# Kernel optimization log

Hardware: AMD Instinct MI355X
Metric: run time of the kernel (lower is better)

Reference implementation:

```python
import jax, jax.numpy as jnp
import numpy as np

NHID, NHEAD, HEAD_DIM, U = 512, 16, 64, 3  # U = unfold_size (hardcoded 3 in original)
B, L = 8, 2048
D = NHEAD * HEAD_DIM  # 1024


def setup_inputs() -> dict:
    key = jax.random.key(0)
    ks = jax.random.split(key, 9)
    s = 0.02
    return {
        "x": jax.random.normal(ks[0], (B, NHID, L, 1), jnp.float32),
        "wq": jax.random.normal(ks[1], (NHID, D), jnp.float32) * s,
        "bq": jnp.zeros((D,), jnp.float32),
        "wk": jax.random.normal(ks[2], (NHID, D), jnp.float32) * s,
        "bk": jnp.zeros((D,), jnp.float32),
        "wv": jax.random.normal(ks[3], (NHID, D), jnp.float32) * s,
        "bv": jnp.zeros((D,), jnp.float32),
        "wo": jax.random.normal(ks[4], (D, NHID), jnp.float32) * s,
        "bo": jnp.zeros((NHID,), jnp.float32),
    }


def _unfold(t):
    # t: (B, D, L). Replicates tf.image.extract_patches (ksize 3, SAME, zero pad)
    # followed by the original's reshape (B,L,1,D,3) -- which reinterprets the
    # window-major flat layout (w*D + c) as (c', w') -- then transpose to
    # (B, D, 3, L) and reshape to (B, nhead, head_dim, 3, L).
    b, d, l = t.shape
    tt = jnp.transpose(t, (0, 2, 1))                  # (B, L, D)
    tp = jnp.pad(tt, ((0, 0), (1, 1), (0, 0)))        # SAME zero padding along L
    p = jnp.stack([tp[:, w:w + l, :] for w in range(U)], axis=2)  # (B, L, 3, D), flat idx = w*D + c
    p = p.reshape(b, l, d, U)                         # faithful reinterpreting reshape
    p = jnp.transpose(p, (0, 2, 3, 1))                # (B, D, 3, L)
    return p.reshape(b, NHEAD, HEAD_DIM, U, l)


def reference(x, wq, bq, wk, bk, wv, bv, wo, bo):
    b, c, l, _ = x.shape
    xs = x[..., 0]                                    # (B, C, L)
    # 1x1 convs (channels_first) == channel matmuls
    q = jnp.einsum('bcl,cd->bdl', xs, wq) + bq[None, :, None]
    k = jnp.einsum('bcl,cd->bdl', xs, wk) + bk[None, :, None]
    v = jnp.einsum('bcl,cd->bdl', xs, wv) + bv[None, :, None]
    q = q.reshape(b, NHEAD, HEAD_DIM, 1, l)           # (B, nh, hd, 1, L)
    k = _unfold(k)                                    # (B, nh, hd, 3, L)
    v = _unfold(v)
    scale = jnp.sqrt(jnp.asarray(HEAD_DIM, x.dtype))
    alphas = jnp.sum(q * k, axis=2, keepdims=True) / scale  # (B, nh, 1, 3, L)
    alphas = jax.nn.softmax(alphas, axis=3)
    att = jnp.sum(alphas * v, axis=3)                 # (B, nh, hd, L)
    # faithful to original: transpose then reinterpreting reshape to (B, D, L)
    att = jnp.transpose(att, (0, 1, 3, 2)).reshape(b, D, l)
    ret = jnp.einsum('bdl,dc->bcl', att, wo) + bo[None, :, None]
    return ret[..., None]                             # (B, nhid, L, 1)
```

## Files before the change

kernel.cpp:

```cpp
#include <hip/hip_runtime.h>

typedef _Float16 f16_t;
typedef _Float16 f16x2 __attribute__((ext_vector_type(2)));
typedef _Float16 f16x8 __attribute__((ext_vector_type(8)));
typedef float floatx4 __attribute__((ext_vector_type(4)));
typedef unsigned int u32;
typedef const __attribute__((address_space(1))) unsigned int* gptr_as1;
typedef __attribute__((address_space(3))) unsigned int* lptr_as3;

#define B_ 8
#define C_ 512
#define L_ 2048
#define D_ 1024
#define H_ 16

static __device__ __forceinline__ f16x2 bc2(u32 v) { return __builtin_bit_cast(f16x2, v); }
static __device__ __forceinline__ u32 cb2(f16x2 v) { return __builtin_bit_cast(u32, v); }

#define SCHEDB() __builtin_amdgcn_sched_barrier(0)

__global__ __launch_bounds__(256) void _MSA1_ktransf2h(const float* __restrict__ in,
                                                       f16_t* __restrict__ out,
                                                       int R, int C) {
  size_t zoff = (size_t)blockIdx.z * R * C;
  in += zoff; out += zoff;
  __shared__ f16_t tile[64][65];
  int r0 = blockIdx.y * 64, c0 = blockIdx.x * 64;
  int t = threadIdx.x;
  #pragma unroll
  for (int i = 0; i < 16; ++i) {
    int idx = t + i * 256;
    int r = idx >> 6, c = idx & 63;
    tile[c][r] = (f16_t)in[(size_t)(r0 + r) * C + (c0 + c)];
  }
  __syncthreads();
  #pragma unroll
  for (int i = 0; i < 16; ++i) {
    int idx = t + i * 256;
    int r = idx >> 6, c = idx & 63;
    out[(size_t)(c0 + r) * R + (r0 + c)] = tile[r][c];
  }
}

__global__ __launch_bounds__(256) void _MSA1_kprep(
    const float* __restrict__ wq, const float* __restrict__ wk,
    const float* __restrict__ wv, const float* __restrict__ wo,
    const float* __restrict__ bq, const float* __restrict__ bk,
    const float* __restrict__ bv,
    f16_t* __restrict__ wT3, f16_t* __restrict__ woT, float* __restrict__ bias3) {
  const int x = blockIdx.x, y = blockIdx.y;
  const int t = threadIdx.x;
  if (x == 128) {
    if (y == 0) {
      for (int i = t; i < 1024; i += 256) {
        bias3[i] = bq[i];
        bias3[1024 + i] = bk[i];
        bias3[2048 + i] = bv[i];
      }
    }
    return;
  }
  __shared__ f16_t tile[64][65];
  const float* in; f16_t* out; int R, C, r0, c0;
  if (y < 3) {
    R = 512; C = 1024;
    in = (y == 0) ? wq : (y == 1) ? wk : wv;
    out = wT3 + (size_t)y * 524288;
    r0 = (x >> 4) * 64; c0 = (x & 15) * 64;
  } else {
    R = 1024; C = 512;
    in = wo; out = woT;
    r0 = (x >> 3) * 64; c0 = (x & 7) * 64;
  }
  #pragma unroll
  for (int i = 0; i < 16; ++i) {
    int idx = t + i * 256;
    int r = idx >> 6, c = idx & 63;
    tile[c][r] = (f16_t)in[(size_t)(r0 + r) * C + (c0 + c)];
  }
  __syncthreads();
  #pragma unroll
  for (int i = 0; i < 16; ++i) {
    int idx = t + i * 256;
    int r = idx >> 6, c = idx & 63;
    out[(size_t)(c0 + r) * R + (r0 + c)] = tile[r][c];
  }
}

template <int K>
__global__ __launch_bounds__(512, 2) void _MSA1_kgemm8(
    const f16_t* __restrict__ A, const f16_t* __restrict__ Bt,
    const float* __restrict__ bias, f16_t* __restrict__ Cd0,
    int M, int N, long sB, long sC) {
  constexpr int KT = K / 64;
  int nx, my, zz;
  if (gridDim.z == 8) {
    const int o = blockIdx.x + 8 * (blockIdx.y + 12 * blockIdx.z);
    zz = o & 7; const int r = o >> 3; nx = r & 7; my = r >> 3;
  } else {
    nx = blockIdx.x; my = blockIdx.y; zz = blockIdx.z;
  }
  const f16_t* Bz = Bt + (size_t)zz * sB;
  const int m0 = my * 256, n0 = nx * 256;

  union __align__(16) ShU {
    f16_t AB[8][8192];
    f16_t Ep[64][264];
  };
  __shared__ ShU sh;

  const int t = threadIdx.x;
  const int lane = t & 63;
  const int wid = t >> 6;
  const int wm = wid & 1, wn = wid >> 1;
  const int mh = wm * 128, nh = wn * 64;
  const int fm = lane & 15, fq = lane >> 4;
  const int srcswz = ((t & 3) ^ ((t >> 2) & 3) ^ ((t >> 4) & 3)) * 8;
  const int colf = ((fq ^ (fm & 3) ^ ((fm >> 2) & 3)) * 8);

  floatx4 acc[8][4];
  #pragma unroll
  for (int i = 0; i < 8; ++i)
    #pragma unroll
    for (int j = 0; j < 4; ++j) {
      floatx4 z4 = {0.f, 0.f, 0.f, 0.f};
      acc[i][j] = z4;
    }

  auto SG = [&](int T, int ab, int kk) {
    const int d = T & 1;
    const f16_t* src = ab ? Bz : A;
    const int base0 = ab ? n0 : m0;
    char* ldsb = (char*)&sh.AB[(d * 2 + ab) * 2 + kk][0];
    #pragma unroll
    for (int j = 0; j < 2; ++j) {
      int idx = j * 512 + t;
      int r = idx >> 2;
      const f16_t* g = src + (size_t)(base0 + r) * K + T * 64 + kk * 32 + srcswz;
      __builtin_amdgcn_global_load_lds((gptr_as1)(const void*)g,
          (lptr_as3)(void*)(ldsb + idx * 16), 16, 0, 0);
    }
  };
  auto LDA4 = [&](f16x8* af, int d, int kk, int mhalf) {
    #pragma unroll
    for (int m2 = 0; m2 < 4; ++m2)
      af[m2] = *(const f16x8*)&sh.AB[(d * 2 + 0) * 2 + kk]
                  [(mh + mhalf * 64 + m2 * 16 + fm) * 32 + colf];
  };
  auto LDB4 = [&](f16x8* bf, int d, int kk) {
    #pragma unroll
    for (int nt = 0; nt < 4; ++nt)
      bf[nt] = *(const f16x8*)&sh.AB[(d * 2 + 1) * 2 + kk]
                  [(nh + nt * 16 + fm) * 32 + colf];
  };
  auto MM = [&](const f16x8* af, const f16x8* bf, int mhalf) {
    __builtin_amdgcn_s_setprio(1);
    #pragma unroll
    for (int m2 = 0; m2 < 4; ++m2)
      #pragma unroll
      for (int nt = 0; nt < 4; ++nt)
        acc[mhalf * 4 + m2][nt] = __builtin_amdgcn_mfma_f32_16x16x32_f16(
            af[m2], bf[nt], acc[mhalf * 4 + m2][nt], 0, 0, 0);
    __builtin_amdgcn_s_setprio(0);
  };

  SG(0, 1, 0); SG(0, 0, 0); SG(0, 1, 1); SG(0, 0, 1);
  SG(1, 1, 0); SG(1, 0, 0); SG(1, 1, 1);
  SCHEDB();
  asm volatile("s_waitcnt vmcnt(10)" ::: "memory");
  __builtin_amdgcn_s_barrier();
  SCHEDB();

  f16x8 af[4], bfr[4];
  #pragma unroll
  for (int i = 0; i < KT; ++i) {
    const int d = i & 1;
    LDB4(bfr, d, 0);
    LDA4(af, d, 0, 0);
    SCHEDB();
    __builtin_amdgcn_s_barrier();
    asm volatile("s_waitcnt lgkmcnt(0)" ::: "memory");
    SCHEDB();
    if (i + 1 < KT) SG(i + 1, 0, 1);
    MM(af, bfr, 0);
    LDA4(af, d, 0, 1);
    SCHEDB();
    if (i == KT - 1) {
      asm volatile("s_waitcnt vmcnt(0)" ::: "memory");
    } else {
      asm volatile("s_waitcnt vmcnt(8)" ::: "memory");
    }
    __builtin_amdgcn_s_barrier();
    asm volatile("s_waitcnt lgkmcnt(0)" ::: "memory");
    SCHEDB();
    if (i + 2 < KT) SG(i + 2, 1, 0);
    MM(af, bfr, 1);
    LDB4(bfr, d, 1);
    LDA4(af, d, 1, 0);
    SCHEDB();
    __builtin_amdgcn_s_barrier();
    asm volatile("s_waitcnt lgkmcnt(0)" ::: "memory");
    SCHEDB();
    if (i + 2 < KT) SG(i + 2, 0, 0);
    MM(af, bfr, 0);
    LDA4(af, d, 1, 1);
    SCHEDB();
    if (i + 1 < KT) {
      asm volatile("s_waitcnt vmcnt(8)" ::: "memory");
    }
    __builtin_amdgcn_s_barrier();
    asm volatile("s_waitcnt lgkmcnt(0)" ::: "memory");
    SCHEDB();
    if (i + 2 < KT) SG(i + 2, 1, 1);
    MM(af, bfr, 1);
  }
  __syncthreads();

  f16_t* Cd = Cd0 + (size_t)zz * sC;
  #pragma unroll
  for (int p = 0; p < 4; ++p) {
    if (p) __syncthreads();
    if (wm == (p >> 1)) {
      #pragma unroll
      for (int m2 = 0; m2 < 4; ++m2) {
        int mt = (p & 1) * 4 + m2;
        float bv4[4];
        #pragma unroll
        for (int r = 0; r < 4; ++r)
          bv4[r] = bias[m0 + p * 64 + m2 * 16 + fq * 4 + r];
        #pragma unroll
        for (int nt = 0; nt < 4; ++nt) {
          int col = nh + nt * 16 + fm;
          #pragma unroll
          for (int r = 0; r < 4; ++r) {
            int row = m2 * 16 + fq * 4 + r;
            sh.Ep[row][col] = (f16_t)(acc[mt][nt][r] + bv4[r]);
          }
        }
      }
    }
    __syncthreads();
    #pragma unroll
    for (int ii = 0; ii < 8; ++ii) {
      int chunk = ii * 512 + t;
      int row = chunk >> 6, c8 = chunk & 63;
      uint2 val = *(const uint2*)&sh.Ep[row][c8 * 4];
      *(uint2*)&Cd[(size_t)(m0 + p * 64 + row) * N + n0 + c8 * 4] = val;
    }
  }
}

template <bool F32OUT, int K>
__global__ __launch_bounds__(512, 2) void _MSA1_kgemm(
    const f16_t* __restrict__ A, const f16_t* __restrict__ Bt,
    const float* __restrict__ bias, void* __restrict__ Cdv,
    int M, int N, long sA, long sB, long sC) {
  int nx, my, zz;
  if (gridDim.z == 8) {
    const int o = blockIdx.x + 16 * (blockIdx.y + 2 * blockIdx.z);
    zz = o & 7; const int r = o >> 3; nx = r & 15; my = r >> 4;
  } else {
    nx = blockIdx.x; my = blockIdx.y; zz = blockIdx.z;
  }
  A  += (size_t)zz * sA;
  Bt += (size_t)zz * sB;
  const int m0 = my * 256, n0 = nx * 128;

  union __align__(16) ShU {
    struct { f16_t As[3][256][32]; f16_t Bs[3][128][32]; } ab;
    f16_t Ep[F32OUT ? 1 : 64][132];
  };
  __shared__ ShU sh;

  const int t = threadIdx.x;
  const int lane = t & 63, w = t >> 6;
  const int mh = (w & 3) * 64, nh = (w >> 2) * 64;
  const int fm = lane & 15, fq = lane >> 4;
  const int srcswz = ((t & 3) ^ ((t >> 2) & 3) ^ ((t >> 4) & 3)) * 8;
  const int colf = ((fq ^ (fm & 3) ^ ((fm >> 2) & 3)) * 8);

  floatx4 acc[4][4];
  #pragma unroll
  for (int i = 0; i < 4; ++i)
    #pragma unroll
    for (int j = 0; j < 4; ++j) {
      floatx4 z4 = {0.f, 0.f, 0.f, 0.f};
      acc[i][j] = z4;
    }

  auto STAGE = [&](int kt, int bi) {
    #pragma unroll
    for (int j = 0; j < 2; ++j) {
      int idx = j * 512 + t;
      int r = idx >> 2;
      const f16_t* ga = A + (size_t)(m0 + r) * K + kt + srcswz;
      __builtin_amdgcn_global_load_lds((gptr_as1)(const void*)ga,
          (lptr_as3)(void*)((char*)&sh.ab.As[bi][0][0] + j * 8192 + w * 1024), 16, 0, 0);
    }
    {
      int r = t >> 2;
      const f16_t* gb = Bt + (size_t)(n0 + r) * K + kt + srcswz;
      __builtin_amdgcn_global_load_lds((gptr_as1)(const void*)gb,
          (lptr_as3)(void*)((char*)&sh.ab.Bs[bi][0][0] + w * 1024), 16, 0, 0);
    }
  };

  STAGE(0, 0);
  STAGE(32, 1);
  SCHEDB();
  asm volatile("s_waitcnt vmcnt(3)" ::: "memory");
  __builtin_amdgcn_s_barrier();
  SCHEDB();

  int bcur = 0;
  for (int kt = 0; kt < K; kt += 32) {
    if (kt + 64 < K) {
      int bi = bcur + 2; if (bi >= 3) bi -= 3;
      STAGE(kt + 64, bi);
    }
    f16x8 af[4], bfr[4];
    #pragma unroll
    for (int mt = 0; mt < 4; ++mt)
      af[mt] = *(const f16x8*)&sh.ab.As[bcur][mh + mt * 16 + fm][colf];
    #pragma unroll
    for (int nt = 0; nt < 4; ++nt)
      bfr[nt] = *(const f16x8*)&sh.ab.Bs[bcur][nh + nt * 16 + fm][colf];
    __builtin_amdgcn_s_setprio(1);
    #pragma unroll
    for (int mt = 0; mt < 4; ++mt)
      #pragma unroll
      for (int nt = 0; nt < 4; ++nt)
        acc[mt][nt] = __builtin_amdgcn_mfma_f32_16x16x32_f16(
            af[mt], bfr[nt], acc[mt][nt], 0, 0, 0);
    __builtin_amdgcn_s_setprio(0);
    if (kt + 32 < K) {
      SCHEDB();
      if (kt + 64 < K)
        asm volatile("s_waitcnt vmcnt(3) lgkmcnt(0)" ::: "memory");
      else
        asm volatile("s_waitcnt vmcnt(0) lgkmcnt(0)" ::: "memory");
      __builtin_amdgcn_s_barrier();
      SCHEDB();
    }
    bcur = (bcur == 2) ? 0 : bcur + 1;
  }
  __syncthreads();

  if (F32OUT) {
    float* Cd = (float*)Cdv + (size_t)zz * sC;
    #pragma unroll
    for (int mt = 0; mt < 4; ++mt) {
      float bv4[4];
      #pragma unroll
      for (int r = 0; r < 4; ++r)
        bv4[r] = bias[m0 + mh + mt * 16 + fq * 4 + r];
      #pragma unroll
      for (int nt = 0; nt < 4; ++nt) {
        int col = n0 + nh + nt * 16 + fm;
        #pragma unroll
        for (int r = 0; r < 4; ++r) {
          int row = m0 + mh + mt * 16 + fq * 4 + r;
          Cd[(size_t)row * N + col] = acc[mt][nt][r] + bv4[r];
        }
      }
    }
  } else {
    f16_t* Cd = (f16_t*)Cdv + (size_t)zz * sC;
    #pragma unroll
    for (int p = 0; p < 4; ++p) {
      if (p) __syncthreads();
      if ((w & 1) == (p >> 1)) {
        #pragma unroll
        for (int mt2 = 0; mt2 < 4; ++mt2) {
          float bv4[4];
          #pragma unroll
          for (int r = 0; r < 4; ++r)
            bv4[r] = bias[m0 + p * 64 + mt2 * 16 + fq * 4 + r];
          #pragma unroll
          for (int nt = 0; nt < 4; ++nt) {
            int col = nh + nt * 16 + fm;
            #pragma unroll
            for (int r = 0; r < 4; ++r) {
              int row = mt2 * 16 + fq * 4 + r;
              sh.Ep[row & (F32OUT ? 0 : 63)][col] = (f16_t)(acc[mt2][nt][r] + bv4[r]);
            }
          }
        }
      }
      __syncthreads();
      #pragma unroll
      for (int i = 0; i < 8; ++i) {
        int chunk = i * 256 + (t & 255);
        int row = chunk >> 5, c8 = chunk & 31;
        uint2 val = *(const uint2*)&sh.Ep[row & (F32OUT ? 0 : 63)][c8 * 4];
        *(uint2*)&Cd[(size_t)(m0 + p * 64 + row) * N + n0 + c8 * 4] = val;
      }
    }
  }
}

__global__ __launch_bounds__(256) void _MSA1_kattn6(const f16_t* __restrict__ qkv,
                                                    f16_t* __restrict__ attT) {
  const int t = threadIdx.x;
  const int lane = t & 63;
  const int wid = __builtin_amdgcn_readfirstlane(t >> 6);
  const int hb = blockIdx.x;
  const int h = hb & 15, b = hb >> 4;
  const int chi = blockIdx.y;
  const int lbase = chi * 256;
  const int l0 = lbase + lane * 4;
  const size_t plane = (size_t)D_ * L_;
  const f16_t* base = qkv + (size_t)b * 3 * plane;

  __shared__ uint2 sred[4][3][64];
  __shared__ __align__(16) f16_t tile2[2048][8];

  const f16_t* qp = base + (size_t)(h * 64 + wid * 16) * L_ + l0;
  const f16_t* kpl = base + plane;
  const f16_t* vpl = base + 2 * plane;
  const int g0 = h * 192 + wid * 48;

  f16x2 sLo[3], sHi[3];
  #pragma unroll
  for (int w = 0; w < 3; ++w) { f16x2 z = {(f16_t)0, (f16_t)0}; sLo[w] = z; sHi[w] = z; }

  #pragma unroll
  for (int dd = 0; dd < 16; ++dd) {
    uint2 qw = *(const uint2*)(qp + (size_t)dd * L_);
    f16x2 qlo = bc2(qw.x), qhi = bc2(qw.y);
    #pragma unroll
    for (int w = 0; w < 3; ++w) {
      int g = g0 + 3 * dd + w;
      int c = g & 1023;
      int o = (g >> 10) - 1;
      uint2 kw = *(const uint2*)(kpl + (size_t)c * L_ + (l0 + o));
      if (o < 0 && l0 == 0) kw.x &= 0xFFFF0000u;
      if (o > 0 && l0 == 2044) kw.y &= 0x0000FFFFu;
      sLo[w] = bc2(kw.x) * qlo + sLo[w];
      sHi[w] = bc2(kw.y) * qhi + sHi[w];
    }
  }
  #pragma unroll
  for (int w = 0; w < 3; ++w) {
    uint2 v; v.x = cb2(sLo[w]); v.y = cb2(sHi[w]);
    sred[wid][w][lane] = v;
  }
  __syncthreads();

  float sc[4][3];
  #pragma unroll
  for (int j = 0; j < 3; ++j) {
    uint2 r0 = sred[0][j][lane], r1 = sred[1][j][lane];
    uint2 r2 = sred[2][j][lane], r3 = sred[3][j][lane];
    f16x2 lo = (bc2(r0.x) + bc2(r1.x)) + (bc2(r2.x) + bc2(r3.x));
    f16x2 hi = (bc2(r0.y) + bc2(r1.y)) + (bc2(r2.y) + bc2(r3.y));
    sc[0][j] = (float)lo.x * 0.125f;
    sc[1][j] = (float)lo.y * 0.125f;
    sc[2][j] = (float)hi.x * 0.125f;
    sc[3][j] = (float)hi.y * 0.125f;
  }
  f16_t ef[4][3];
  #pragma unroll
  for (int li = 0; li < 4; ++li) {
    float mx = fmaxf(sc[li][0], fmaxf(sc[li][1], sc[li][2]));
    float e0 = __expf(sc[li][0] - mx), e1 = __expf(sc[li][1] - mx), e2 = __expf(sc[li][2] - mx);
    float inv = 1.f / (e0 + e1 + e2);
    ef[li][0] = (f16_t)(e0 * inv); ef[li][1] = (f16_t)(e1 * inv); ef[li][2] = (f16_t)(e2 * inv);
  }
  f16x2 eLo[3], eHi[3];
  #pragma unroll
  for (int w = 0; w < 3; ++w) {
    f16x2 a = {ef[0][w], ef[1][w]}; eLo[w] = a;
    f16x2 b2 = {ef[2][w], ef[3][w]}; eHi[w] = b2;
  }

  const int llb = (lane & 7) * 256 + wid * 16;
  const int jcol = lane >> 3;
  #pragma unroll
  for (int dd = 0; dd < 16; ++dd) {
    f16x2 aLo = {(f16_t)0, (f16_t)0}, aHi = {(f16_t)0, (f16_t)0};
    #pragma unroll
    for (int w = 0; w < 3; ++w) {
      int g = g0 + 3 * dd + w;
      int c = g & 1023;
      int o = (g >> 10) - 1;
      uint2 vw = *(const uint2*)(vpl + (size_t)c * L_ + (l0 + o));
      if (o < 0 && l0 == 0) vw.x &= 0xFFFF0000u;
      if (o > 0 && l0 == 2044) vw.y &= 0x0000FFFFu;
      aLo = bc2(vw.x) * eLo[w] + aLo;
      aHi = bc2(vw.y) * eHi[w] + aHi;
    }
    const int llq = llb + dd;
    tile2[llq +   0][jcol] = aLo.x;
    tile2[llq +  64][jcol] = aLo.y;
    tile2[llq + 128][jcol] = aHi.x;
    tile2[llq + 192][jcol] = aHi.y;
  }
  __syncthreads();

  f16_t* ob = attT + (size_t)b * L_ * D_ + h * 64 + chi * 8;
  #pragma unroll
  for (int i = 0; i < 8; ++i) {
    int ll = i * 256 + t;
    uint4 val = *(const uint4*)&tile2[ll][0];
    *(uint4*)(ob + (size_t)ll * D_) = val;
  }
}

extern "C" void kernel_launch(void* const* d_in, const int* in_sizes, int n_in,
                              void* d_out, int out_size, void* d_ws, size_t ws_size,
                              hipStream_t stream) {
  (void)in_sizes; (void)n_in; (void)out_size;
  const float* x  = (const float*)d_in[0];
  const float* wq = (const float*)d_in[1];
  const float* bq = (const float*)d_in[2];
  const float* wk = (const float*)d_in[3];
  const float* bk = (const float*)d_in[4];
  const float* wv = (const float*)d_in[5];
  const float* bv = (const float*)d_in[6];
  const float* wo = (const float*)d_in[7];
  const float* bo = (const float*)d_in[8];
  float* out = (float*)d_out;
  char* ws = (char*)d_ws;

  f16_t* wT3   = (f16_t*)(ws);
  f16_t* woT   = (f16_t*)(ws + 3145728);
  float* bias3 = (float*) (ws + 4194304);
  const size_t SHARED_END = 4210688;

  _MSA1_kprep<<<dim3(129, 4), dim3(256), 0, stream>>>(
      wq, wk, wv, wo, bq, bk, bv, wT3, woT, bias3);

  if (ws_size >= 155205632ull) {
    f16_t* xT    = (f16_t*)(ws + SHARED_END);
    f16_t* qkv   = xT + 8388608ull;
    f16_t* att2T = qkv + 50331648ull;

    _MSA1_ktransf2h<<<dim3(32, 8, B_), dim3(256), 0, stream>>>(x, xT, 512, 2048);
    _MSA1_kgemm8<512><<<dim3(8, 12, B_), dim3(512), 0, stream>>>(
        wT3, xT, bias3, qkv, 3072, 2048,
        (long)(2048 * 512), (long)(3072 * 2048));
    _MSA1_kattn6<<<dim3(128, 8), dim3(256), 0, stream>>>(qkv, att2T);
    _MSA1_kgemm<true, 1024><<<dim3(16, 2, B_), dim3(512), 0, stream>>>(
        woT, att2T, bo, out, 512, 2048,
        0L, (long)(2048 * 1024), (long)(512 * 2048));
  } else {
    f16_t* xTb    = (f16_t*)(ws + SHARED_END);
    f16_t* qkvb   = xTb + 1048576ull;
    f16_t* att2Tb = qkvb + 6291456ull;
    for (int b = 0; b < B_; ++b) {
      const float* xb = x + (size_t)b * C_ * L_;
      _MSA1_ktransf2h<<<dim3(32, 8, 1), dim3(256), 0, stream>>>(xb, xTb, 512, 2048);
      _MSA1_kgemm8<512><<<dim3(8, 12, 1), dim3(512), 0, stream>>>(
          wT3, xTb, bias3, qkvb, 3072, 2048, 0L, 0L);
      _MSA1_kattn6<<<dim3(16, 8), dim3(256), 0, stream>>>(qkvb, att2Tb);
      _MSA1_kgemm<true, 1024><<<dim3(16, 2, 1), dim3(512), 0, stream>>>(
          woT, att2Tb, bo, out + (size_t)b * C_ * L_, 512, 2048, 0L, 0L, 0L);
    }
  }
}
```

Measured before the change: 256.6 us.

## Replace QKV GEMM's 256x256 hand-pipelined kernel with 128x256 triple-buffered tiles

The QKV projection GEMM drops its 256x256 tile with the hand-scheduled double-buffered pipeline and uses a 128x256 tile. Its main loop is now a simpler triple-buffered 32-wide K loop modeled on the output GEMM, with occupancy hint 4 and twice as many blocks in the grid. The XCD-aware block-index remapping is removed from both GEMMs. The aim is more resident waves and better latency hiding, at the cost of lower per-block data reuse, more global/LDS traffic per FLOP, and worse L2 locality without the remap.

```diff
diff --git a/kernel.cpp b/kernel.cpp
--- a/kernel.cpp
+++ b/kernel.cpp
@@ -88,220 +88,50 @@
 }
 
 template <int K>
-__global__ __launch_bounds__(512, 2) void _MSA1_kgemm8(
+__global__ __launch_bounds__(512, 4) void _MSA1_kgemm8(
     const f16_t* __restrict__ A, const f16_t* __restrict__ Bt,
     const float* __restrict__ bias, f16_t* __restrict__ Cd0,
     int M, int N, long sB, long sC) {
-  constexpr int KT = K / 64;
-  int nx, my, zz;
-  if (gridDim.z == 8) {
-    const int o = blockIdx.x + 8 * (blockIdx.y + 12 * blockIdx.z);
-    zz = o & 7; const int r = o >> 3; nx = r & 7; my = r >> 3;
-  } else {
-    nx = blockIdx.x; my = blockIdx.y; zz = blockIdx.z;
-  }
-  const f16_t* Bz = Bt + (size_t)zz * sB;
-  const int m0 = my * 256, n0 = nx * 256;
+  const f16_t* Bz = Bt + (size_t)blockIdx.z * sB;
+  const int m0 = blockIdx.y * 128, n0 = blockIdx.x * 256;
 
   union __align__(16) ShU {
-    f16_t AB[8][8192];
+    struct { f16_t As[3][128][32]; f16_t Bs[3][256][32]; } ab;
     f16_t Ep[64][264];
   };
   __shared__ ShU sh;
 
   const int t = threadIdx.x;
-  const int lane = t & 63;
-  const int wid = t >> 6;
-  const int wm = wid & 1, wn = wid >> 1;
-  const int mh = wm * 128, nh = wn * 64;
+  const int lane = t & 63, w = t >> 6;
+  const int wm = w & 1;
+  const int mh = wm * 64, nh = (w >> 1) * 64;
   const int fm = lane & 15, fq = lane >> 4;
   const int srcswz = ((t & 3) ^ ((t >> 2) & 3) ^ ((t >> 4) & 3)) * 8;
   const int colf = ((fq ^ (fm & 3) ^ ((fm >> 2) & 3)) * 8);
 
-  floatx4 acc[8][4];
-  #pragma unroll
-  for (int i = 0; i < 8; ++i)
+  floatx4 acc[4][4];
+  #pragma unroll
+  for (int i = 0; i < 4; ++i)
     #pragma unroll
     for (int j = 0; j < 4; ++j) {
       floatx4 z4 = {0.f, 0.f, 0.f, 0.f};
       acc[i][j] = z4;
     }
 
-  auto SG = [&](int T, int ab, int kk) {
-    const int d = T & 1;
-    const f16_t* src = ab ? Bz : A;
-    const int base0 = ab ? n0 : m0;
-    char* ldsb = (char*)&sh.AB[(d * 2 + ab) * 2 + kk][0];
+  auto STAGE = [&](int kt, int bi) {
+    {
+      int r = t >> 2;
+      const f16_t* ga = A + (size_t)(m0 + r) * K + kt + srcswz;
+      __builtin_amdgcn_global_load_lds((gptr_as1)(const void*)ga,
+          (lptr_as3)(void*)((char*)&sh.ab.As[bi][0][0] + t * 16), 16, 0, 0);
+    }
     #pragma unroll
     for (int j = 0; j < 2; ++j) {
       int idx = j * 512 + t;
       int r = idx >> 2;
-      const f16_t* g = src + (size_t)(base0 + r) * K + T * 64 + kk * 32 + srcswz;
-      __builtin_amdgcn_global_load_lds((gptr_as1)(const void*)g,
-          (lptr_as3)(void*)(ldsb + idx * 16), 16, 0, 0);
-    }
-  };
-  auto LDA4 = [&](f16x8* af, int d, int kk, int mhalf) {
-    #pragma unroll
-    for (int m2 = 0; m2 < 4; ++m2)
-      af[m2] = *(const f16x8*)&sh.AB[(d * 2 + 0) * 2 + kk]
-                  [(mh + mhalf * 64 + m2 * 16 + fm) * 32 + colf];
-  };
-  auto LDB4 = [&](f16x8* bf, int d, int kk) {
-    #pragma unroll
-    for (int nt = 0; nt < 4; ++nt)
-      bf[nt] = *(const f16x8*)&sh.AB[(d * 2 + 1) * 2 + kk]
-                  [(nh + nt * 16 + fm) * 32 + colf];
-  };
-  auto MM = [&](const f16x8* af, const f16x8* bf, int mhalf) {
-    __builtin_amdgcn_s_setprio(1);
-    #pragma unroll
-    for (int m2 = 0; m2 < 4; ++m2)
-      #pragma unroll
-      for (int nt = 0; nt < 4; ++nt)
-        acc[mhalf * 4 + m2][nt] = __builtin_amdgcn_mfma_f32_16x16x32_f16(
-            af[m2], bf[nt], acc[mhalf * 4 + m2][nt], 0, 0, 0);
-    __builtin_amdgcn_s_setprio(0);
-  };
-
-  SG(0, 1, 0); SG(0, 0, 0); SG(0, 1, 1); SG(0, 0, 1);
-  SG(1, 1, 0); SG(1, 0, 0); SG(1, 1, 1);
-  SCHEDB();
-  asm volatile("s_waitcnt vmcnt(10)" ::: "memory");
-  __builtin_amdgcn_s_barrier();
-  SCHEDB();
-
-  f16x8 af[4], bfr[4];
-  #pragma unroll
-  for (int i = 0; i < KT; ++i) {
-    const int d = i & 1;
-    LDB4(bfr, d, 0);
-    LDA4(af, d, 0, 0);
-    SCHEDB();
-    __builtin_amdgcn_s_barrier();
-    asm volatile("s_waitcnt lgkmcnt(0)" ::: "memory");
-    SCHEDB();
-    if (i + 1 < KT) SG(i + 1, 0, 1);
-    MM(af, bfr, 0);
-    LDA4(af, d, 0, 1);
-    SCHEDB();
-    if (i == KT - 1) {
-      asm volatile("s_waitcnt vmcnt(0)" ::: "memory");
-    } else {
-      asm volatile("s_waitcnt vmcnt(8)" ::: "memory");
-    }
-    __builtin_amdgcn_s_barrier();
-    asm volatile("s_waitcnt lgkmcnt(0)" ::: "memory");
-    SCHEDB();
-    if (i + 2 < KT) SG(i + 2, 1, 0);
-    MM(af, bfr, 1);
-    LDB4(bfr, d, 1);
-    LDA4(af, d, 1, 0);
-    SCHEDB();
-    __builtin_amdgcn_s_barrier();
-    asm volatile("s_waitcnt lgkmcnt(0)" ::: "memory");
-    SCHEDB();
-    if (i + 2 < KT) SG(i + 2, 0, 0);
-    MM(af, bfr, 0);
-    LDA4(af, d, 1, 1);
-    SCHEDB();
-    if (i + 1 < KT) {
-      asm volatile("s_waitcnt vmcnt(8)" ::: "memory");
-    }
-    __builtin_amdgcn_s_barrier();
-    asm volatile("s_waitcnt lgkmcnt(0)" ::: "memory");
-    SCHEDB();
-    if (i + 2 < KT) SG(i + 2, 1, 1);
-    MM(af, bfr, 1);
-  }
-  __syncthreads();
-
-  f16_t* Cd = Cd0 + (size_t)zz * sC;
-  #pragma unroll
-  for (int p = 0; p < 4; ++p) {
-    if (p) __syncthreads();
-    if (wm == (p >> 1)) {
-      #pragma unroll
-      for (int m2 = 0; m2 < 4; ++m2) {
-        int mt = (p & 1) * 4 + m2;
-        float bv4[4];
-        #pragma unroll
-        for (int r = 0; r < 4; ++r)
-          bv4[r] = bias[m0 + p * 64 + m2 * 16 + fq * 4 + r];
-        #pragma unroll
-        for (int nt = 0; nt < 4; ++nt) {
-          int col = nh + nt * 16 + fm;
-          #pragma unroll
-          for (int r = 0; r < 4; ++r) {
-            int row = m2 * 16 + fq * 4 + r;
-            sh.Ep[row][col] = (f16_t)(acc[mt][nt][r] + bv4[r]);
-          }
-        }
-      }
-    }
-    __syncthreads();
-    #pragma unroll
-    for (int ii = 0; ii < 8; ++ii) {
-      int chunk = ii * 512 + t;
-      int row = chunk >> 6, c8 = chunk & 63;
-      uint2 val = *(const uint2*)&sh.Ep[row][c8 * 4];
-      *(uint2*)&Cd[(size_t)(m0 + p * 64 + row) * N + n0 + c8 * 4] = val;
-    }
-  }
-}
-
-template <bool F32OUT, int K>
-__global__ __launch_bounds__(512, 2) void _MSA1_kgemm(
-    const f16_t* __restrict__ A, const f16_t* __restrict__ Bt,
-    const float* __restrict__ bias, void* __restrict__ Cdv,
-    int M, int N, long sA, long sB, long sC) {
-  int nx, my, zz;
-  if (gridDim.z == 8) {
-    const int o = blockIdx.x + 16 * (blockIdx.y + 2 * blockIdx.z);
-    zz = o & 7; const int r = o >> 3; nx = r & 15; my = r >> 4;
-  } else {
-    nx = blockIdx.x; my = blockIdx.y; zz = blockIdx.z;
-  }
-  A  += (size_t)zz * sA;
-  Bt += (size_t)zz * sB;
-  const int m0 = my * 256, n0 = nx * 128;
-
-  union __align__(16) ShU {
-    struct { f16_t As[3][256][32]; f16_t Bs[3][128][32]; } ab;
-    f16_t Ep[F32OUT ? 1 : 64][132];
-  };
-  __shared__ ShU sh;
-
-  const int t = threadIdx.x;
-  const int lane = t & 63, w = t >> 6;
-  const int mh = (w & 3) * 64, nh = (w >> 2) * 64;
-  const int fm = lane & 15, fq = lane >> 4;
-  const int srcswz = ((t & 3) ^ ((t >> 2) & 3) ^ ((t >> 4) & 3)) * 8;
-  const int colf = ((fq ^ (fm & 3) ^ ((fm >> 2) & 3)) * 8);
-
-  floatx4 acc[4][4];
-  #pragma unroll
-  for (int i = 0; i < 4; ++i)
-    #pragma unroll
-    for (int j = 0; j < 4; ++j) {
-      floatx4 z4 = {0.f, 0.f, 0.f, 0.f};
-      acc[i][j] = z4;
-    }
-
-  auto STAGE = [&](int kt, int bi) {
-    #pragma unroll
-    for (int j = 0; j < 2; ++j) {
-      int idx = j * 512 + t;
-      int r = idx >> 2;
-      const f16_t* ga = A + (size_t)(m0 + r) * K + kt + srcswz;
-      __builtin_amdgcn_global_load_lds((gptr_as1)(const void*)ga,
-          (lptr_as3)(void*)((char*)&sh.ab.As[bi][0][0] + j * 8192 + w * 1024), 16, 0, 0);
-    }
-    {
-      int r = t >> 2;
-      const f16_t* gb = Bt + (size_t)(n0 + r) * K + kt + srcswz;
+      const f16_t* gb = Bz + (size_t)(n0 + r) * K + kt + srcswz;
       __builtin_amdgcn_global_load_lds((gptr_as1)(const void*)gb,
-          (lptr_as3)(void*)((char*)&sh.ab.Bs[bi][0][0] + w * 1024), 16, 0, 0);
+          (lptr_as3)(void*)((char*)&sh.ab.Bs[bi][0][0] + idx * 16), 16, 0, 0);
     }
   };
 
@@ -346,8 +176,130 @@
   }
   __syncthreads();
 
+  f16_t* Cd = Cd0 + (size_t)blockIdx.z * sC;
+  #pragma unroll
+  for (int p = 0; p < 2; ++p) {
+    if (p) __syncthreads();
+    if (wm == p) {
+      #pragma unroll
+      for (int mt = 0; mt < 4; ++mt) {
+        float bv4[4];
+        #pragma unroll
+        for (int r = 0; r < 4; ++r)
+          bv4[r] = bias[m0 + p * 64 + mt * 16 + fq * 4 + r];
+        #pragma unroll
+        for (int nt = 0; nt < 4; ++nt) {
+          int col = nh + nt * 16 + fm;
+          #pragma unroll
+          for (int r = 0; r < 4; ++r) {
+            int row = mt * 16 + fq * 4 + r;
+            sh.Ep[row][col] = (f16_t)(acc[mt][nt][r] + bv4[r]);
+          }
+        }
+      }
+    }
+    __syncthreads();
+    #pragma unroll
+    for (int ii = 0; ii < 8; ++ii) {
+      int chunk = ii * 512 + t;
+      int row = chunk >> 6, c8 = chunk & 63;
+      uint2 val = *(const uint2*)&sh.Ep[row][c8 * 4];
+      *(uint2*)&Cd[(size_t)(m0 + p * 64 + row) * N + n0 + c8 * 4] = val;
+    }
+  }
+}
+
+template <bool F32OUT, int K>
+__global__ __launch_bounds__(512, 2) void _MSA1_kgemm(
+    const f16_t* __restrict__ A, const f16_t* __restrict__ Bt,
+    const float* __restrict__ bias, void* __restrict__ Cdv,
+    int M, int N, long sA, long sB, long sC) {
+  A  += (size_t)blockIdx.z * sA;
+  Bt += (size_t)blockIdx.z * sB;
+  const int m0 = blockIdx.y * 256, n0 = blockIdx.x * 128;
+
+  union __align__(16) ShU {
+    struct { f16_t As[3][256][32]; f16_t Bs[3][128][32]; } ab;
+    f16_t Ep[F32OUT ? 1 : 64][132];
+  };
+  __shared__ ShU sh;
+
+  const int t = threadIdx.x;
+  const int lane = t & 63, w = t >> 6;
+  const int mh = (w & 3) * 64, nh = (w >> 2) * 64;
+  const int fm = lane & 15, fq = lane >> 4;
+  const int srcswz = ((t & 3) ^ ((t >> 2) & 3) ^ ((t >> 4) & 3)) * 8;
+  const int colf = ((fq ^ (fm & 3) ^ ((fm >> 2) & 3)) * 8);
+
+  floatx4 acc[4][4];
+  #pragma unroll
+  for (int i = 0; i < 4; ++i)
+    #pragma unroll
+    for (int j = 0; j < 4; ++j) {
+      floatx4 z4 = {0.f, 0.f, 0.f, 0.f};
+      acc[i][j] = z4;
+    }
+
+  auto STAGE = [&](int kt, int bi) {
+    #pragma unroll
+    for (int j = 0; j < 2; ++j) {
+      int idx = j * 512 + t;
+      int r = idx >> 2;
+      const f16_t* ga = A + (size_t)(m0 + r) * K + kt + srcswz;
+      __builtin_amdgcn_global_load_lds((gptr_as1)(const void*)ga,
+          (lptr_as3)(void*)((char*)&sh.ab.As[bi][0][0] + idx * 16), 16, 0, 0);
+    }
+    {
+      int r = t >> 2;
+      const f16_t* gb = Bt + (size_t)(n0 + r) * K + kt + srcswz;
+      __builtin_amdgcn_global_load_lds((gptr_as1)(const void*)gb,
+          (lptr_as3)(void*)((char*)&sh.ab.Bs[bi][0][0] + t * 16), 16, 0, 0);
+    }
+  };
+
+  STAGE(0, 0);
+  STAGE(32, 1);
+  SCHEDB();
+  asm volatile("s_waitcnt vmcnt(3)" ::: "memory");
+  __builtin_amdgcn_s_barrier();
+  SCHEDB();
+
+  int bcur = 0;
+  for (int kt = 0; kt < K; kt += 32) {
+    if (kt + 64 < K) {
+      int bi = bcur + 2; if (bi >= 3) bi -= 3;
+      STAGE(kt + 64, bi);
+    }
+    f16x8 af[4], bfr[4];
+    #pragma unroll
+    for (int mt = 0; mt < 4; ++mt)
+      af[mt] = *(const f16x8*)&sh.ab.As[bcur][mh + mt * 16 + fm][colf];
+    #pragma unroll
+    for (int nt = 0; nt < 4; ++nt)
+      bfr[nt] = *(const f16x8*)&sh.ab.Bs[bcur][nh + nt * 16 + fm][colf];
+    __builtin_amdgcn_s_setprio(1);
+    #pragma unroll
+    for (int mt = 0; mt < 4; ++mt)
+      #pragma unroll
+      for (int nt = 0; nt < 4; ++nt)
+        acc[mt][nt] = __builtin_amdgcn_mfma_f32_16x16x32_f16(
+            af[mt], bfr[nt], acc[mt][nt], 0, 0, 0);
+    __builtin_amdgcn_s_setprio(0);
+    if (kt + 32 < K) {
+      SCHEDB();
+      if (kt + 64 < K)
+        asm volatile("s_waitcnt vmcnt(3) lgkmcnt(0)" ::: "memory");
+      else
+        asm volatile("s_waitcnt vmcnt(0) lgkmcnt(0)" ::: "memory");
+      __builtin_amdgcn_s_barrier();
+      SCHEDB();
+    }
+    bcur = (bcur == 2) ? 0 : bcur + 1;
+  }
+  __syncthreads();
+
   if (F32OUT) {
-    float* Cd = (float*)Cdv + (size_t)zz * sC;
+    float* Cd = (float*)Cdv + (size_t)blockIdx.z * sC;
     #pragma unroll
     for (int mt = 0; mt < 4; ++mt) {
       float bv4[4];
@@ -365,7 +317,7 @@
       }
     }
   } else {
-    f16_t* Cd = (f16_t*)Cdv + (size_t)zz * sC;
+    f16_t* Cd = (f16_t*)Cdv + (size_t)blockIdx.z * sC;
     #pragma unroll
     for (int p = 0; p < 4; ++p) {
       if (p) __syncthreads();
@@ -537,7 +489,7 @@
     f16_t* att2T = qkv + 50331648ull;
 
     _MSA1_ktransf2h<<<dim3(32, 8, B_), dim3(256), 0, stream>>>(x, xT, 512, 2048);
-    _MSA1_kgemm8<512><<<dim3(8, 12, B_), dim3(512), 0, stream>>>(
+    _MSA1_kgemm8<512><<<dim3(8, 24, B_), dim3(512), 0, stream>>>(
         wT3, xT, bias3, qkv, 3072, 2048,
         (long)(2048 * 512), (long)(3072 * 2048));
     _MSA1_kattn6<<<dim3(128, 8), dim3(256), 0, stream>>>(qkv, att2T);
@@ -551,7 +503,7 @@
     for (int b = 0; b < B_; ++b) {
       const float* xb = x + (size_t)b * C_ * L_;
       _MSA1_ktransf2h<<<dim3(32, 8, 1), dim3(256), 0, stream>>>(xb, xTb, 512, 2048);
-      _MSA1_kgemm8<512><<<dim3(8, 12, 1), dim3(512), 0, stream>>>(
+      _MSA1_kgemm8<512><<<dim3(8, 24, 1), dim3(512), 0, stream>>>(
           wT3, xTb, bias3, qkvb, 3072, 2048, 0L, 0L);
       _MSA1_kattn6<<<dim3(16, 8), dim3(256), 0, stream>>>(qkvb, att2Tb);
       _MSA1_kgemm<true, 1024><<<dim3(16, 2, 1), dim3(512), 0, stream>>>(
```

After: 254.0 us. No clear change (-1.0%).
